# Kernel optimization log

Hardware: AMD Instinct MI355X
Metric: run time of the kernel (lower is better)

Reference implementation:

```python
import jax, jax.numpy as jnp
import numpy as np

NUM_CODEBOOKS = 32
CODEBOOK_DIM = 128
NUM_VECTORS = 16384
NUM_CENTROIDS = 256


def setup_inputs() -> dict:
    key = jax.random.key(0)
    k_idx, k_cb = jax.random.split(key)
    indices = jax.random.randint(k_idx, (NUM_CODEBOOKS, NUM_VECTORS), 0, NUM_CENTROIDS, dtype=jnp.int32)
    codebooks = jax.random.normal(k_cb, (NUM_CODEBOOKS, NUM_CENTROIDS, CODEBOOK_DIM), dtype=jnp.float32)
    return {"indices": indices, "codebooks": codebooks}


def reference(indices, codebooks) -> jnp.ndarray:
    # Per-codebook gather: w[h, c, :] = codebooks[h, indices[h, c], :]
    h = jnp.arange(codebooks.shape[0])[:, None]          # (H, 1)
    w = codebooks[h, indices]                            # (H, C, D)
    # rearrange 'h c d -> c (h d)'
    H, C, D = w.shape
    return jnp.transpose(w, (1, 0, 2)).reshape(C, H * D)  # (num_vectors, H*D)
```

## Files before the change

### kernel.cpp

```cpp
#include <hip/hip_runtime.h>


#define RPQ_H  32
#define RPQ_C  16384
#define RPQ_D  128
#define RPQ_NC 256

__global__ void rpq_gather_kernel(const int* __restrict__ indices,
                                  const float* __restrict__ codebooks,
                                  float* __restrict__ out) {
    const float4* __restrict__ cb = reinterpret_cast<const float4*>(codebooks);
    float4* __restrict__ o = reinterpret_cast<float4*>(out);

    const unsigned total = (unsigned)RPQ_C * (RPQ_H * RPQ_D / 4);

    for (unsigned v = blockIdx.x * blockDim.x + threadIdx.x; v < total;
         v += gridDim.x * blockDim.x) {
        const unsigned c   = v >> 10;
        const unsigned rem = v & 1023u;
        const unsigned h   = rem >> 5;
        const unsigned d4  = rem & 31u;

        const int idx = indices[h * RPQ_C + c];
        o[v] = cb[((h << 8) + (unsigned)idx) * 32u + d4];
    }
}

extern "C" void kernel_launch(void* const* d_in, const int* in_sizes, int n_in,
                              void* d_out, int out_size, void* d_ws, size_t ws_size,
                              hipStream_t stream) {
    const int*   indices   = (const int*)d_in[0];
    const float* codebooks = (const float*)d_in[1];
    float*       out       = (float*)d_out;

    const int block = 256;
    const int grid  = 2048;
    rpq_gather_kernel<<<grid, block, 0, stream>>>(indices, codebooks, out);
}
```

Measured before the change: 59.63 us.

## Stage per-codebook table and indices in LDS and gather from shared memory

Replaces the grid-stride global gather with one block per (codebook, 1024-row slice). Each block copies that codebook's full 128 KB table and its 1024 indices into LDS, then each wave writes 512-byte output segments read from LDS. This is meant to remove repeated global and L2 reads of codebook rows and index values. In exchange, every block reloads its table, which adds about 64 MB of reads in total. The large LDS footprint limits each CU to one 1024-thread block, and output writes become strided 512-byte chunks instead of fully contiguous rows.

Result: faster. 54.74 us (-8.2%).

```diff
diff --git a/kernel.cpp b/kernel.cpp
--- a/kernel.cpp
+++ b/kernel.cpp
@@ -6,23 +6,51 @@
 #define RPQ_D  128
 #define RPQ_NC 256
 
-__global__ void rpq_gather_kernel(const int* __restrict__ indices,
-                                  const float* __restrict__ codebooks,
-                                  float* __restrict__ out) {
-    const float4* __restrict__ cb = reinterpret_cast<const float4*>(codebooks);
-    float4* __restrict__ o = reinterpret_cast<float4*>(out);
+#define BLOCK        1024
+#define CBLK_PER_H   16
+#define ROWS_PER_BLK (RPQ_C / CBLK_PER_H)
+#define GRID         (RPQ_H * CBLK_PER_H)
 
-    const unsigned total = (unsigned)RPQ_C * (RPQ_H * RPQ_D / 4);
+#define CB_F4_PER_H  (RPQ_NC * RPQ_D / 4)
+#define LDS_CB_BYTES (CB_F4_PER_H * 16)
+#define LDS_IDX_BYTES (ROWS_PER_BLK * 4)
+#define LDS_BYTES    (LDS_CB_BYTES + LDS_IDX_BYTES)
 
-    for (unsigned v = blockIdx.x * blockDim.x + threadIdx.x; v < total;
-         v += gridDim.x * blockDim.x) {
-        const unsigned c   = v >> 10;
-        const unsigned rem = v & 1023u;
-        const unsigned h   = rem >> 5;
-        const unsigned d4  = rem & 31u;
+#define ROW_F4       (RPQ_H * RPQ_D / 4)
 
-        const int idx = indices[h * RPQ_C + c];
-        o[v] = cb[((h << 8) + (unsigned)idx) * 32u + d4];
+typedef float f4 __attribute__((ext_vector_type(4)));
+
+__global__ __launch_bounds__(BLOCK) void rpq_lds_kernel(
+        const int* __restrict__ indices,
+        const float* __restrict__ codebooks,
+        float* __restrict__ out) {
+    extern __shared__ char smem[];
+    f4*  lds_cb  = reinterpret_cast<f4*>(smem);
+    int* lds_idx = reinterpret_cast<int*>(smem + LDS_CB_BYTES);
+
+    const unsigned bid    = blockIdx.x;
+    const unsigned h      = bid >> 4;
+    const unsigned cblk   = bid & 15u;
+    const unsigned c_base = cblk * ROWS_PER_BLK;
+    const unsigned tid    = threadIdx.x;
+
+    const f4* cb4 = reinterpret_cast<const f4*>(codebooks) + (size_t)h * CB_F4_PER_H;
+#pragma unroll
+    for (int k = 0; k < 8; ++k)
+        lds_cb[tid + k * BLOCK] = cb4[tid + k * BLOCK];
+    lds_idx[tid] = indices[h * RPQ_C + c_base + tid];
+    __syncthreads();
+
+    const unsigned d4 = tid & 31u;
+    const unsigned r0 = tid >> 5;
+    f4* o = reinterpret_cast<f4*>(out)
+            + (size_t)(c_base + r0) * ROW_F4 + h * (RPQ_D / 4) + d4;
+
+#pragma unroll 4
+    for (int it = 0; it < ROWS_PER_BLK / 32; ++it) {
+        const int idx = lds_idx[it * 32 + r0];
+        const f4  v   = lds_cb[(unsigned)idx * 32u + d4];
+        o[(size_t)it * 32u * ROW_F4] = v;
     }
 }
 
@@ -33,7 +61,8 @@
     const float* codebooks = (const float*)d_in[1];
     float*       out       = (float*)d_out;
 
-    const int block = 256;
-    const int grid  = 2048;
-    rpq_gather_kernel<<<grid, block, 0, stream>>>(indices, codebooks, out);
+    hipFuncSetAttribute((const void*)rpq_lds_kernel,
+                        hipFuncAttributeMaxDynamicSharedMemorySize, LDS_BYTES);
+
+    rpq_lds_kernel<<<GRID, BLOCK, LDS_BYTES, stream>>>(indices, codebooks, out);
 }
```
